# Optimization experiments

Hardware: AMD Instinct MI355X
Metric: run time of the kernel (lower is better)

## Reference

```python
import jax, jax.numpy as jnp
import numpy as np

N_NODES = 100000
N_EDGES = 1500000
N_REL = 3
HID = 256


def setup_inputs() -> dict:
    key = jax.random.key(0)
    ks = jax.random.split(key, 8)
    return {
        "feat_a": jax.random.normal(ks[0], (N_NODES, 256), dtype=jnp.float32),
        "feat_b": jax.random.normal(ks[1], (N_NODES, 384), dtype=jnp.float32),
        "Wp_a": jax.random.normal(ks[2], (256, HID), dtype=jnp.float32) * 0.03,
        "Wp_b": jax.random.normal(ks[3], (384, HID), dtype=jnp.float32) * 0.03,
        "Wr": jax.random.normal(ks[4], (N_REL, HID, HID), dtype=jnp.float32) * 0.06,
        "ln_gamma": jnp.ones((HID,), dtype=jnp.float32),
        "ln_beta": jnp.zeros((HID,), dtype=jnp.float32),
        "edge_weight": jax.random.uniform(ks[5], (N_EDGES,), dtype=jnp.float32),
        "edge_src": jax.random.randint(ks[6], (N_EDGES,), 0, N_NODES, dtype=jnp.int32),
        "edge_dst": jax.random.randint(ks[7], (N_EDGES,), 0, N_NODES, dtype=jnp.int32),
    }


def _layer_norm(x, gamma, beta, eps=1e-5):
    mu = jnp.mean(x, axis=-1, keepdims=True)
    var = jnp.mean(jnp.square(x - mu), axis=-1, keepdims=True)
    return (x - mu) * jax.lax.rsqrt(var + eps) * gamma + beta


def reference(feat_a, feat_b, Wp_a, Wp_b, Wr, ln_gamma, ln_beta,
              edge_weight, edge_src, edge_dst):
    # avg fusion of modality projections (bias-free linears), padding node zeroed
    h0 = 0.5 * (feat_a @ Wp_a + feat_b @ Wp_b)  # [N, H]
    h0 = h0.at[0].set(0.0)

    n = h0.shape[0]
    e_per_rel = edge_src.shape[0] // N_REL  # edges pre-sorted by relation id
    aggregated = jnp.zeros_like(h0)
    for r in range(N_REL):
        s = slice(r * e_per_rel, (r + 1) * e_per_rel)
        src, dst, w = edge_src[s], edge_dst[s], edge_weight[s]
        # gather -> relation linear -> weight scale  [E_r, H]
        msg = (h0[src] @ Wr[r]) * w[:, None]
        num = jax.ops.segment_sum(msg, dst, num_segments=n)
        den = jax.ops.segment_sum(w, dst, num_segments=n)
        aggregated = aggregated + num / jnp.maximum(den, 1e-8)[:, None]

    # dropout p=0 / eval -> identity; residual + LayerNorm, padding node zeroed
    h1 = _layer_norm(h0 + aggregated, ln_gamma, ln_beta)
    h1 = h1.at[0].set(0.0)
    return h1
```

## Files before the change

kernel.cpp:

```cpp
#include <hip/hip_runtime.h>

#define N_NODES 100000
#define HID 256
#define N_EDGES 1500000
#define N_REL 3
#define E_PER_REL (N_EDGES / N_REL)
#define NKEYS (N_REL * N_NODES)
#define KP 640
#define KR 768

#define SCAN_CHUNK 1024
#define NSCANBLK ((NKEYS + SCAN_CHUNK - 1) / SCAN_CHUNK)

typedef __attribute__((ext_vector_type(8))) short bf16x8;
typedef __attribute__((ext_vector_type(4))) float f32x4;

__device__ __forceinline__ short f2bf(float x) {
    union { float f; unsigned u; } v; v.f = x;
    unsigned r = v.u + 0x7fffu + ((v.u >> 16) & 1u);
    return (short)(r >> 16);
}
__device__ __forceinline__ float bf2f(short h) {
    union { unsigned u; float f; } v;
    v.u = ((unsigned)(unsigned short)h) << 16;
    return v.f;
}
__device__ __forceinline__ int xorf(int r) { return (r & 3) ^ ((r >> 2) & 3); }

__global__ __launch_bounds__(256) void wprep_kernel(
    const float* __restrict__ Wa, const float* __restrict__ Wb,
    const float* __restrict__ Wr,
    short* __restrict__ WTp, short* __restrict__ WTr)
{
    int idx = blockIdx.x * 256 + threadIdx.x;
    if (idx < 256 * KP) {
        int c = idx / KP, k = idx - c * KP;
        float v = (k < 256) ? Wa[k * HID + c] : Wb[(k - 256) * HID + c];
        WTp[idx] = f2bf(0.5f * v);
    } else {
        int j = idx - 256 * KP;
        if (j < 256 * KR) {
            int c = j / KR, k = j - c * KR;
            WTr[j] = f2bf(Wr[(k >> 8) * HID * HID + (k & 255) * HID + c]);
        }
    }
}

__global__ __launch_bounds__(512, 4) void proj_gemm(
    const float* __restrict__ fa, const float* __restrict__ fb,
    const short* __restrict__ WTp, short* __restrict__ h0h)
{
    __shared__ short smA[128 * 32];
    __shared__ short smB[256 * 32];
    const int tid = threadIdx.x;
    const int lane = tid & 63;
    const int w = tid >> 6;
    const int wr = w >> 2, wc = w & 3;
    const int brow = blockIdx.x * 128;

    f32x4 acc[4][4] = {};

    const int arow = tid >> 2;
    const int akq = tid & 3;
    int garow = brow + arow;
    if (garow >= N_NODES) garow = N_NODES - 1;
    const int aslot = akq ^ xorf(arow);
    const int bcol = tid >> 1;
    const int bkh = tid & 1;
    const int bs0 = (2 * bkh + 0) ^ xorf(bcol);
    const int bs1 = (2 * bkh + 1) ^ xorf(bcol);

    f32x4 pa0, pa1;
    bf16x8 pb0, pb1;
    auto loadA = [&](int k0) {
        const float* asrc; int astr, kk;
        if (k0 < 256) { asrc = fa; astr = 256; kk = k0; }
        else          { asrc = fb; astr = 384; kk = k0 - 256; }
        const float* ap = asrc + (size_t)garow * astr + kk + akq * 8;
        pa0 = *(const f32x4*)(ap + 0);
        pa1 = *(const f32x4*)(ap + 4);
    };
    auto loadB = [&](int k0) {
        const short* bp = WTp + (size_t)bcol * KP + k0 + bkh * 16;
        pb0 = *(const bf16x8*)(bp + 0);
        pb1 = *(const bf16x8*)(bp + 8);
    };

    loadA(0); loadB(0);
    for (int k0 = 0; k0 < KP; k0 += 32) {
        __syncthreads();
        bf16x8 ha;
        ha[0] = f2bf(pa0.x); ha[1] = f2bf(pa0.y); ha[2] = f2bf(pa0.z); ha[3] = f2bf(pa0.w);
        ha[4] = f2bf(pa1.x); ha[5] = f2bf(pa1.y); ha[6] = f2bf(pa1.z); ha[7] = f2bf(pa1.w);
        *(bf16x8*)((char*)smA + arow * 64 + aslot * 16) = ha;
        *(bf16x8*)((char*)smB + bcol * 64 + bs0 * 16) = pb0;
        *(bf16x8*)((char*)smB + bcol * 64 + bs1 * 16) = pb1;
        __syncthreads();
        if (k0 + 32 < KP) { loadA(k0 + 32); loadB(k0 + 32); }

        bf16x8 afr[4], bfr[4];
        #pragma unroll
        for (int m = 0; m < 4; ++m) {
            int rt = wr * 64 + m * 16 + (lane & 15);
            int s = (lane >> 4) ^ xorf(rt);
            afr[m] = *(const bf16x8*)((const char*)smA + rt * 64 + s * 16);
        }
        #pragma unroll
        for (int n = 0; n < 4; ++n) {
            int ct = wc * 64 + n * 16 + (lane & 15);
            int s = (lane >> 4) ^ xorf(ct);
            bfr[n] = *(const bf16x8*)((const char*)smB + ct * 64 + s * 16);
        }
        #pragma unroll
        for (int m = 0; m < 4; ++m)
            #pragma unroll
            for (int n = 0; n < 4; ++n)
                acc[m][n] = __builtin_amdgcn_mfma_f32_16x16x32_bf16(
                    afr[m], bfr[n], acc[m][n], 0, 0, 0);
    }

    #pragma unroll
    for (int m = 0; m < 4; ++m) {
        #pragma unroll
        for (int j = 0; j < 4; ++j) {
            int row = brow + wr * 64 + m * 16 + ((lane >> 4) << 2) + j;
            if (row >= N_NODES) continue;
            #pragma unroll
            for (int n = 0; n < 4; ++n) {
                int col = wc * 64 + n * 16 + (lane & 15);
                short v = (row == 0) ? (short)0 : f2bf(acc[m][n][j]);
                h0h[(size_t)row * HID + col] = v;
            }
        }
    }
}

__global__ __launch_bounds__(512, 4) void rel_gemm_ln(
    const short* __restrict__ S, const short* __restrict__ WTr,
    const short* __restrict__ h0h,
    const float* __restrict__ gamma, const float* __restrict__ beta,
    float* __restrict__ out)
{
    __shared__ short smA[128 * 32];
    __shared__ short smB[256 * 32];
    __shared__ float redS[128][4];
    __shared__ float redS2[128][4];
    __shared__ float smMean[128], smRs[128];
    __shared__ float smG[256], smBt[256];
    const int tid = threadIdx.x;
    const int lane = tid & 63;
    const int w = tid >> 6;
    const int wr = w >> 2, wc = w & 3;
    const int brow = blockIdx.x * 128;

    if (tid < 256) { smG[tid] = gamma[tid]; smBt[tid] = beta[tid]; }

    f32x4 acc[4][4] = {};

    const int arow = tid >> 2;
    const int akq = tid & 3;
    int garow = brow + arow;
    if (garow >= N_NODES) garow = N_NODES - 1;
    const int aslot = akq ^ xorf(arow);
    const int bcol = tid >> 1;
    const int bkh = tid & 1;
    const int bs0 = (2 * bkh + 0) ^ xorf(bcol);
    const int bs1 = (2 * bkh + 1) ^ xorf(bcol);

    bf16x8 pa, pb0, pb1;
    auto loadA = [&](int k0) {
        pa = *(const bf16x8*)(S + (size_t)garow * KR + k0 + akq * 8);
    };
    auto loadB = [&](int k0) {
        const short* bp = WTr + (size_t)bcol * KR + k0 + bkh * 16;
        pb0 = *(const bf16x8*)(bp + 0);
        pb1 = *(const bf16x8*)(bp + 8);
    };

    loadA(0); loadB(0);
    for (int k0 = 0; k0 < KR; k0 += 32) {
        __syncthreads();
        *(bf16x8*)((char*)smA + arow * 64 + aslot * 16) = pa;
        *(bf16x8*)((char*)smB + bcol * 64 + bs0 * 16) = pb0;
        *(bf16x8*)((char*)smB + bcol * 64 + bs1 * 16) = pb1;
        __syncthreads();
        if (k0 + 32 < KR) { loadA(k0 + 32); loadB(k0 + 32); }

        bf16x8 afr[4], bfr[4];
        #pragma unroll
        for (int m = 0; m < 4; ++m) {
            int rt = wr * 64 + m * 16 + (lane & 15);
            int s = (lane >> 4) ^ xorf(rt);
            afr[m] = *(const bf16x8*)((const char*)smA + rt * 64 + s * 16);
        }
        #pragma unroll
        for (int n = 0; n < 4; ++n) {
            int ct = wc * 64 + n * 16 + (lane & 15);
            int s = (lane >> 4) ^ xorf(ct);
            bfr[n] = *(const bf16x8*)((const char*)smB + ct * 64 + s * 16);
        }
        #pragma unroll
        for (int m = 0; m < 4; ++m)
            #pragma unroll
            for (int n = 0; n < 4; ++n)
                acc[m][n] = __builtin_amdgcn_mfma_f32_16x16x32_bf16(
                    afr[m], bfr[n], acc[m][n], 0, 0, 0);
    }

    #pragma unroll
    for (int m = 0; m < 4; ++m) {
        #pragma unroll
        for (int j = 0; j < 4; ++j) {
            int lrow = wr * 64 + m * 16 + ((lane >> 4) << 2) + j;
            int grow = brow + lrow;
            int crow = (grow < N_NODES) ? grow : 0;
            float s = 0.f, s2 = 0.f;
            #pragma unroll
            for (int n = 0; n < 4; ++n) {
                int col = wc * 64 + n * 16 + (lane & 15);
                float x = acc[m][n][j] + bf2f(h0h[(size_t)crow * HID + col]);
                acc[m][n][j] = x;
                s += x; s2 = fmaf(x, x, s2);
            }
            #pragma unroll
            for (int off = 1; off < 16; off <<= 1) {
                s += __shfl_xor(s, off, 64);
                s2 += __shfl_xor(s2, off, 64);
            }
            if ((lane & 15) == 0) { redS[lrow][wc] = s; redS2[lrow][wc] = s2; }
        }
    }
    __syncthreads();
    if (tid < 128) {
        float tot  = redS[tid][0] + redS[tid][1] + redS[tid][2] + redS[tid][3];
        float tot2 = redS2[tid][0] + redS2[tid][1] + redS2[tid][2] + redS2[tid][3];
        float mean = tot * (1.0f / HID);
        float var = tot2 * (1.0f / HID) - mean * mean;
        smMean[tid] = mean;
        smRs[tid] = rsqrtf(var + 1e-5f);
    }
    __syncthreads();
    #pragma unroll
    for (int m = 0; m < 4; ++m) {
        #pragma unroll
        for (int j = 0; j < 4; ++j) {
            int lrow = wr * 64 + m * 16 + ((lane >> 4) << 2) + j;
            int grow = brow + lrow;
            if (grow >= N_NODES) continue;
            float mean = smMean[lrow], rs = smRs[lrow];
            #pragma unroll
            for (int n = 0; n < 4; ++n) {
                int col = wc * 64 + n * 16 + (lane & 15);
                float y = (acc[m][n][j] - mean) * rs * smG[col] + smBt[col];
                out[(size_t)grow * HID + col] = (grow == 0) ? 0.f : y;
            }
        }
    }
}

__global__ __launch_bounds__(256) void hist_kernel(
    const int* __restrict__ dst, int* __restrict__ count)
{
    int i = blockIdx.x * 256 + threadIdx.x;
    if (i >= N_EDGES) return;
    int r = i / E_PER_REL;
    atomicAdd(&count[r * N_NODES + dst[i]], 1);
}

__global__ __launch_bounds__(256) void scan1_kernel(
    const int* __restrict__ count, int* __restrict__ offset,
    int* __restrict__ bsum)
{
    __shared__ int tmp[256];
    const int t = threadIdx.x;
    const int base = blockIdx.x * SCAN_CHUNK + t * 4;
    int v[4];
    #pragma unroll
    for (int j = 0; j < 4; ++j)
        v[j] = (base + j < NKEYS) ? count[base + j] : 0;
    int tsum = v[0] + v[1] + v[2] + v[3];
    tmp[t] = tsum;
    __syncthreads();
    #pragma unroll
    for (int off = 1; off < 256; off <<= 1) {
        int x = (t >= off) ? tmp[t - off] : 0;
        __syncthreads();
        tmp[t] += x;
        __syncthreads();
    }
    int run = tmp[t] - tsum;
    #pragma unroll
    for (int j = 0; j < 4; ++j) {
        if (base + j < NKEYS) offset[base + j] = run;
        run += v[j];
    }
    if (t == 0) bsum[blockIdx.x] = tmp[255];
}

__global__ __launch_bounds__(256) void scan2_kernel(int* __restrict__ bsum)
{
    __shared__ int tmp[256];
    const int t = threadIdx.x;
    int v0 = (2 * t     < NSCANBLK) ? bsum[2 * t]     : 0;
    int v1 = (2 * t + 1 < NSCANBLK) ? bsum[2 * t + 1] : 0;
    int psum = v0 + v1;
    tmp[t] = psum;
    __syncthreads();
    #pragma unroll
    for (int off = 1; off < 256; off <<= 1) {
        int x = (t >= off) ? tmp[t - off] : 0;
        __syncthreads();
        tmp[t] += x;
        __syncthreads();
    }
    int excl = tmp[t] - psum;
    if (2 * t     < NSCANBLK) bsum[2 * t]     = excl;
    if (2 * t + 1 < NSCANBLK) bsum[2 * t + 1] = excl + v0;
}

__global__ __launch_bounds__(256) void scan3_kernel(
    int* __restrict__ offset, const int* __restrict__ bsum)
{
    int i = blockIdx.x * 256 + threadIdx.x;
    if (i >= NKEYS) return;
    offset[i] += bsum[i / SCAN_CHUNK];
}

__global__ __launch_bounds__(256) void fill_kernel(
    const int* __restrict__ src, const int* __restrict__ dst,
    const float* __restrict__ w,
    int* __restrict__ offset, int* __restrict__ csr_src,
    float* __restrict__ csr_w)
{
    int i = blockIdx.x * 256 + threadIdx.x;
    if (i >= N_EDGES) return;
    int r = i / E_PER_REL;
    int key = r * N_NODES + dst[i];
    int pos = atomicAdd(&offset[key], 1);
    csr_src[pos] = src[i];
    csr_w[pos] = w[i];
}

__global__ __launch_bounds__(256) void gather_kernel(
    const short* __restrict__ h0h,
    const int* __restrict__ ends, const int* __restrict__ count,
    const int* __restrict__ csr_src, const float* __restrict__ csr_w,
    short* __restrict__ S)
{
    int gw = (blockIdx.x * 256 + threadIdx.x) >> 6;
    int lane = threadIdx.x & 63;
    if (gw >= N_REL * N_NODES) return;
    int r = gw / N_NODES;
    int node = gw - r * N_NODES;
    int deg = count[gw];
    int end = ends[gw];
    int start = end - deg;
    const size_t colo = (size_t)lane * 4;

    float a0 = 0.f, a1 = 0.f, a2 = 0.f, a3 = 0.f;
    float den = 0.f;

    if (deg > 0) {
        int degc = (deg < 64) ? deg : 64;
        int myp = start + ((lane < degc) ? lane : 0);
        int msrc = csr_src[myp];
        float mw = (lane < degc) ? csr_w[myp] : 0.f;

        for (int p = 0; p < degc; p += 4) {
            #pragma unroll
            for (int j = 0; j < 4; ++j) {
                int q = p + j;
                bool ok = q < degc;
                int sj = __shfl(msrc, ok ? q : 0, 64);
                float wj = ok ? __shfl(mw, q, 64) : 0.f;
                short4 v = *(const short4*)(h0h + (size_t)sj * HID + colo);
                a0 = fmaf(wj, bf2f(v.x), a0);
                a1 = fmaf(wj, bf2f(v.y), a1);
                a2 = fmaf(wj, bf2f(v.z), a2);
                a3 = fmaf(wj, bf2f(v.w), a3);
                den += wj;
            }
        }
        for (int p = start + 64; p < end; ++p) {
            int s = csr_src[p];
            float wt = csr_w[p];
            short4 v = *(const short4*)(h0h + (size_t)s * HID + colo);
            a0 = fmaf(wt, bf2f(v.x), a0);
            a1 = fmaf(wt, bf2f(v.y), a1);
            a2 = fmaf(wt, bf2f(v.z), a2);
            a3 = fmaf(wt, bf2f(v.w), a3);
            den += wt;
        }
    }

    float inv = 1.0f / fmaxf(den, 1e-8f);
    short4 o;
    o.x = f2bf(a0 * inv);
    o.y = f2bf(a1 * inv);
    o.z = f2bf(a2 * inv);
    o.w = f2bf(a3 * inv);
    *(short4*)(S + (size_t)node * KR + r * HID + colo) = o;
}

extern "C" void kernel_launch(void* const* d_in, const int* in_sizes, int n_in,
                              void* d_out, int out_size, void* d_ws, size_t ws_size,
                              hipStream_t stream) {
    const float* fa    = (const float*)d_in[0];
    const float* fb    = (const float*)d_in[1];
    const float* Wa    = (const float*)d_in[2];
    const float* Wb    = (const float*)d_in[3];
    const float* Wr    = (const float*)d_in[4];
    const float* gamma = (const float*)d_in[5];
    const float* beta  = (const float*)d_in[6];
    const float* ew    = (const float*)d_in[7];
    const int*   esrc  = (const int*)d_in[8];
    const int*   edst  = (const int*)d_in[9];
    float* out = (float*)d_out;

    char* ws = (char*)d_ws;
    size_t off = 0;
    short* h0h     = (short*)(ws + off); off += (size_t)N_NODES * HID * 2;
    short* S       = (short*)(ws + off); off += (size_t)N_NODES * KR * 2;
    short* WTp     = (short*)(ws + off); off += (size_t)256 * KP * 2;
    short* WTr     = (short*)(ws + off); off += (size_t)256 * KR * 2;
    int*   count   = (int*)  (ws + off); off += (size_t)NKEYS * 4;
    int*   offs    = (int*)  (ws + off); off += (size_t)NKEYS * 4;
    int*   bsum    = (int*)  (ws + off); off += 4096;
    int*   csr_src = (int*)  (ws + off); off += (size_t)N_EDGES * 4;
    float* csr_w   = (float*)(ws + off); off += (size_t)N_EDGES * 4;

    wprep_kernel<<<(256 * KP + 256 * KR) / 256, 256, 0, stream>>>(
        Wa, Wb, Wr, WTp, WTr);

    const int ngrid = (N_NODES + 127) / 128;
    proj_gemm<<<ngrid, 512, 0, stream>>>(fa, fb, WTp, h0h);

    hipMemsetAsync(count, 0, (size_t)NKEYS * 4, stream);
    const int egrid = (N_EDGES + 255) / 256;
    hist_kernel<<<egrid, 256, 0, stream>>>(edst, count);
    scan1_kernel<<<NSCANBLK, 256, 0, stream>>>(count, offs, bsum);
    scan2_kernel<<<1, 256, 0, stream>>>(bsum);
    scan3_kernel<<<(NKEYS + 255) / 256, 256, 0, stream>>>(offs, bsum);
    fill_kernel<<<egrid, 256, 0, stream>>>(esrc, edst, ew, offs, csr_src, csr_w);

    gather_kernel<<<(N_REL * N_NODES * 64) / 256, 256, 0, stream>>>(
        h0h, offs, count, csr_src, csr_w, S);

    rel_gemm_ln<<<ngrid, 512, 0, stream>>>(S, WTr, h0h, gamma, beta, out);
}
```

Baseline: 527.4 us.

## Double-buffer GEMM tiles with direct global-to-LDS loads

Result: no change. 527.7 us (+0.0%).

```diff
diff --git a/kernel.cpp b/kernel.cpp
--- a/kernel.cpp
+++ b/kernel.cpp
@@ -26,6 +26,12 @@
     return v.f;
 }
 __device__ __forceinline__ int xorf(int r) { return (r & 3) ^ ((r >> 2) & 3); }
+
+__device__ __forceinline__ void gload16(const void* g, void* l) {
+    typedef const __attribute__((address_space(1))) unsigned int gq;
+    typedef __attribute__((address_space(3))) unsigned int lq;
+    __builtin_amdgcn_global_load_lds((gq*)g, (lq*)l, 16, 0, 0);
+}
 
 __global__ __launch_bounds__(256) void wprep_kernel(
     const float* __restrict__ Wa, const float* __restrict__ Wb,
@@ -50,8 +56,8 @@
     const float* __restrict__ fa, const float* __restrict__ fb,
     const short* __restrict__ WTp, short* __restrict__ h0h)
 {
-    __shared__ short smA[128 * 32];
-    __shared__ short smB[256 * 32];
+    __shared__ float smA[2][128 * 32];
+    __shared__ short smB[2][256 * 32];
     const int tid = threadIdx.x;
     const int lane = tid & 63;
     const int w = tid >> 6;
@@ -60,56 +66,63 @@
 
     f32x4 acc[4][4] = {};
 
-    const int arow = tid >> 2;
-    const int akq = tid & 3;
-    int garow = brow + arow;
-    if (garow >= N_NODES) garow = N_NODES - 1;
-    const int aslot = akq ^ xorf(arow);
-    const int bcol = tid >> 1;
-    const int bkh = tid & 1;
-    const int bs0 = (2 * bkh + 0) ^ xorf(bcol);
-    const int bs1 = (2 * bkh + 1) ^ xorf(bcol);
-
-    f32x4 pa0, pa1;
-    bf16x8 pb0, pb1;
-    auto loadA = [&](int k0) {
+    const int a_r8 = lane >> 3;
+    const int a_sl = (lane & 7) ^ a_r8;
+    const int b_c16 = lane >> 2;
+
+    int aRowG[2], bColL[2], bSl[2];
+    #pragma unroll
+    for (int ii = 0; ii < 2; ++ii) {
+        int i = w * 2 + ii;
+        int gr = brow + i * 8 + a_r8;
+        aRowG[ii] = (gr < N_NODES) ? gr : (N_NODES - 1);
+        bColL[ii] = i * 16 + b_c16;
+        bSl[ii] = (lane & 3) ^ xorf(bColL[ii]);
+    }
+
+    auto stage = [&](int buf, int k0) {
         const float* asrc; int astr, kk;
         if (k0 < 256) { asrc = fa; astr = 256; kk = k0; }
         else          { asrc = fb; astr = 384; kk = k0 - 256; }
-        const float* ap = asrc + (size_t)garow * astr + kk + akq * 8;
-        pa0 = *(const f32x4*)(ap + 0);
-        pa1 = *(const f32x4*)(ap + 4);
+        #pragma unroll
+        for (int ii = 0; ii < 2; ++ii) {
+            int i = w * 2 + ii;
+            gload16(asrc + (size_t)aRowG[ii] * astr + kk + a_sl * 4,
+                    (char*)&smA[buf][0] + i * 1024);
+        }
+        #pragma unroll
+        for (int ii = 0; ii < 2; ++ii) {
+            int i = w * 2 + ii;
+            gload16(WTp + (size_t)bColL[ii] * KP + k0 + bSl[ii] * 8,
+                    (char*)&smB[buf][0] + i * 1024);
+        }
     };
-    auto loadB = [&](int k0) {
-        const short* bp = WTp + (size_t)bcol * KP + k0 + bkh * 16;
-        pb0 = *(const bf16x8*)(bp + 0);
-        pb1 = *(const bf16x8*)(bp + 8);
-    };
-
-    loadA(0); loadB(0);
-    for (int k0 = 0; k0 < KP; k0 += 32) {
-        __syncthreads();
-        bf16x8 ha;
-        ha[0] = f2bf(pa0.x); ha[1] = f2bf(pa0.y); ha[2] = f2bf(pa0.z); ha[3] = f2bf(pa0.w);
-        ha[4] = f2bf(pa1.x); ha[5] = f2bf(pa1.y); ha[6] = f2bf(pa1.z); ha[7] = f2bf(pa1.w);
-        *(bf16x8*)((char*)smA + arow * 64 + aslot * 16) = ha;
-        *(bf16x8*)((char*)smB + bcol * 64 + bs0 * 16) = pb0;
-        *(bf16x8*)((char*)smB + bcol * 64 + bs1 * 16) = pb1;
-        __syncthreads();
-        if (k0 + 32 < KP) { loadA(k0 + 32); loadB(k0 + 32); }
+
+    stage(0, 0);
+    __syncthreads();
+    int cur = 0;
+    for (int t = 0; t < KP / 32; ++t) {
+        int knext = (t + 1) * 32;
+        if (knext < KP) stage(cur ^ 1, knext);
 
         bf16x8 afr[4], bfr[4];
         #pragma unroll
         for (int m = 0; m < 4; ++m) {
             int rt = wr * 64 + m * 16 + (lane & 15);
-            int s = (lane >> 4) ^ xorf(rt);
-            afr[m] = *(const bf16x8*)((const char*)smA + rt * 64 + s * 16);
+            int p0 = (((lane >> 4) << 1) | 0) ^ (rt & 7);
+            int p1 = (((lane >> 4) << 1) | 1) ^ (rt & 7);
+            f32x4 lo = *(const f32x4*)((const char*)&smA[cur][0] + rt * 128 + p0 * 16);
+            f32x4 hi = *(const f32x4*)((const char*)&smA[cur][0] + rt * 128 + p1 * 16);
+            bf16x8 tb;
+            tb[0] = f2bf(lo.x); tb[1] = f2bf(lo.y); tb[2] = f2bf(lo.z); tb[3] = f2bf(lo.w);
+            tb[4] = f2bf(hi.x); tb[5] = f2bf(hi.y); tb[6] = f2bf(hi.z); tb[7] = f2bf(hi.w);
+            afr[m] = tb;
         }
         #pragma unroll
         for (int n = 0; n < 4; ++n) {
             int ct = wc * 64 + n * 16 + (lane & 15);
-            int s = (lane >> 4) ^ xorf(ct);
-            bfr[n] = *(const bf16x8*)((const char*)smB + ct * 64 + s * 16);
+            int p = (lane >> 4) ^ xorf(ct);
+            bfr[n] = *(const bf16x8*)((const char*)&smB[cur][0] + ct * 64 + p * 16);
         }
         #pragma unroll
         for (int m = 0; m < 4; ++m)
@@ -117,6 +130,9 @@
             for (int n = 0; n < 4; ++n)
                 acc[m][n] = __builtin_amdgcn_mfma_f32_16x16x32_bf16(
                     afr[m], bfr[n], acc[m][n], 0, 0, 0);
+
+        __syncthreads();
+        cur ^= 1;
     }
 
     #pragma unroll
@@ -141,8 +157,8 @@
     const float* __restrict__ gamma, const float* __restrict__ beta,
     float* __restrict__ out)
 {
-    __shared__ short smA[128 * 32];
-    __shared__ short smB[256 * 32];
+    __shared__ short smA[2][128 * 32];
+    __shared__ short smB[2][256 * 32];
     __shared__ float redS[128][4];
     __shared__ float redS2[128][4];
     __shared__ float smMean[128], smRs[128];
@@ -157,47 +173,50 @@
 
     f32x4 acc[4][4] = {};
 
-    const int arow = tid >> 2;
-    const int akq = tid & 3;
-    int garow = brow + arow;
-    if (garow >= N_NODES) garow = N_NODES - 1;
-    const int aslot = akq ^ xorf(arow);
-    const int bcol = tid >> 1;
-    const int bkh = tid & 1;
-    const int bs0 = (2 * bkh + 0) ^ xorf(bcol);
-    const int bs1 = (2 * bkh + 1) ^ xorf(bcol);
-
-    bf16x8 pa, pb0, pb1;
-    auto loadA = [&](int k0) {
-        pa = *(const bf16x8*)(S + (size_t)garow * KR + k0 + akq * 8);
+    const int s_r16 = lane >> 2;
+    const int sRowL = w * 16 + s_r16;
+    int gr0 = brow + sRowL;
+    const int sRowG = (gr0 < N_NODES) ? gr0 : (N_NODES - 1);
+    const int sSl = (lane & 3) ^ xorf(sRowL);
+    const int b_c16 = lane >> 2;
+    int bColL[2], bSl[2];
+    #pragma unroll
+    for (int ii = 0; ii < 2; ++ii) {
+        int i = w * 2 + ii;
+        bColL[ii] = i * 16 + b_c16;
+        bSl[ii] = (lane & 3) ^ xorf(bColL[ii]);
+    }
+
+    auto stage = [&](int buf, int k0) {
+        gload16(S + (size_t)sRowG * KR + k0 + sSl * 8,
+                (char*)&smA[buf][0] + w * 1024);
+        #pragma unroll
+        for (int ii = 0; ii < 2; ++ii) {
+            int i = w * 2 + ii;
+            gload16(WTr + (size_t)bColL[ii] * KR + k0 + bSl[ii] * 8,
+                    (char*)&smB[buf][0] + i * 1024);
+        }
     };
-    auto loadB = [&](int k0) {
-        const short* bp = WTr + (size_t)bcol * KR + k0 + bkh * 16;
-        pb0 = *(const bf16x8*)(bp + 0);
-        pb1 = *(const bf16x8*)(bp + 8);
-    };
-
-    loadA(0); loadB(0);
-    for (int k0 = 0; k0 < KR; k0 += 32) {
-        __syncthreads();
-        *(bf16x8*)((char*)smA + arow * 64 + aslot * 16) = pa;
-        *(bf16x8*)((char*)smB + bcol * 64 + bs0 * 16) = pb0;
-        *(bf16x8*)((char*)smB + bcol * 64 + bs1 * 16) = pb1;
-        __syncthreads();
-        if (k0 + 32 < KR) { loadA(k0 + 32); loadB(k0 + 32); }
+
+    stage(0, 0);
+    __syncthreads();
+    int cur = 0;
+    for (int t = 0; t < KR / 32; ++t) {
+        int knext = (t + 1) * 32;
+        if (knext < KR) stage(cur ^ 1, knext);
 
         bf16x8 afr[4], bfr[4];
         #pragma unroll
         for (int m = 0; m < 4; ++m) {
             int rt = wr * 64 + m * 16 + (lane & 15);
-            int s = (lane >> 4) ^ xorf(rt);
-            afr[m] = *(const bf16x8*)((const char*)smA + rt * 64 + s * 16);
+            int p = (lane >> 4) ^ xorf(rt);
+            afr[m] = *(const bf16x8*)((const char*)&smA[cur][0] + rt * 64 + p * 16);
         }
         #pragma unroll
         for (int n = 0; n < 4; ++n) {
             int ct = wc * 64 + n * 16 + (lane & 15);
-            int s = (lane >> 4) ^ xorf(ct);
-            bfr[n] = *(const bf16x8*)((const char*)smB + ct * 64 + s * 16);
+            int p = (lane >> 4) ^ xorf(ct);
+            bfr[n] = *(const bf16x8*)((const char*)&smB[cur][0] + ct * 64 + p * 16);
         }
         #pragma unroll
         for (int m = 0; m < 4; ++m)
@@ -205,6 +224,9 @@
             for (int n = 0; n < 4; ++n)
                 acc[m][n] = __builtin_amdgcn_mfma_f32_16x16x32_bf16(
                     afr[m], bfr[n], acc[m][n], 0, 0, 0);
+
+        __syncthreads();
+        cur ^= 1;
     }
 
     #pragma unroll
```
